# Optimization experiments

Measured on AMD Instinct MI355X. Metric: run time of the kernel, lower is better.

Reference implementation:

```python
import jax, jax.numpy as jnp
import numpy as np

# dims: L=tgt len, S=src len, N=batch, E=embed, H=heads
L, S, N, E, H = 1024, 1024, 4, 1024, 16
HD = E // H  # head dim = 64


def setup_inputs() -> dict:
    key = jax.random.key(0)
    ks = jax.random.split(key, 7)
    w_scale = 0.02
    return {
        "query": jax.random.normal(ks[0], (L, N, E), jnp.float32),
        "key": jax.random.normal(ks[1], (S, N, E), jnp.float32),
        "value": jax.random.normal(ks[2], (S, N, E), jnp.float32),
        "in_proj_weight": jax.random.normal(ks[3], (3 * E, E), jnp.float32) * w_scale,
        "in_proj_bias": jax.random.normal(ks[4], (3 * E,), jnp.float32) * w_scale,
        "out_proj_weight": jax.random.normal(ks[5], (E, E), jnp.float32) * w_scale,
        "out_proj_bias": jax.random.normal(ks[6], (E,), jnp.float32) * w_scale,
    }


def reference(query, key, value, in_proj_weight, in_proj_bias,
              out_proj_weight, out_proj_bias):
    scaling = float(HD) ** -0.5
    # packed QKV projection, sliced exactly as the torch code does
    q = (query @ in_proj_weight[:E].T + in_proj_bias[:E]) * scaling        # (L,N,E)
    k = key @ in_proj_weight[E:2 * E].T + in_proj_bias[E:2 * E]            # (S,N,E)
    v = value @ in_proj_weight[2 * E:].T + in_proj_bias[2 * E:]            # (S,N,E)
    # split heads: (L,N,E) -> (N*H, L, HD)
    q = q.reshape(L, N * H, HD).transpose(1, 0, 2)
    k = k.reshape(S, N * H, HD).transpose(1, 0, 2)
    v = v.reshape(S, N * H, HD).transpose(1, 0, 2)
    scores = jnp.einsum('bld,bsd->bls', q, k)          # (N*H, L, S)
    attn = jax.nn.softmax(scores, axis=-1)
    sig = jax.nn.sigmoid(scores)                        # the need_sigmoid_weights variant
    out = jnp.einsum('bls,bsd->bld', attn, v)          # (N*H, L, HD)
    out = out.transpose(1, 0, 2).reshape(L, N, E)
    out = out @ out_proj_weight.T + out_proj_bias       # (L,N,E)
    # weights averaged over heads, as torch MHA returns: (N,L,S)
    attn_weights = attn.reshape(N, H, L, S).sum(axis=1) / H
    sig_weights = sig.reshape(N, H, L, S).sum(axis=1) / H
    return out, attn_weights, sig_weights
```

## Files before the change

kernel.cpp:

```cpp
#include <hip/hip_runtime.h>

#define L_DIM 1024
#define E_DIM 1024
#define NB 4
#define H_NUM 16
#define HD_DIM 64
#define T_TOK 4096
#define NHB 64

typedef float f32x4 __attribute__((ext_vector_type(4)));
typedef unsigned short u16x8 __attribute__((ext_vector_type(8)));
typedef unsigned short u16x4 __attribute__((ext_vector_type(4)));
typedef __bf16 bf16x8 __attribute__((ext_vector_type(8)));

__device__ inline unsigned short f2bf(float f) {
  unsigned int u = __builtin_bit_cast(unsigned int, f);
  u += 0x7FFFu + ((u >> 16) & 1u);
  return (unsigned short)(u >> 16);
}
__device__ __forceinline__ unsigned int cvt_pk_bf16(float lo, float hi) {
  unsigned int r;
  asm("v_cvt_pk_bf16_f32 %0, %1, %2" : "=v"(r) : "v"(lo), "v"(hi));
  return r;
}
__device__ inline f32x4 mfma16(u16x8 a, u16x8 b, f32x4 c) {
  return __builtin_amdgcn_mfma_f32_16x16x32_bf16(
      __builtin_bit_cast(bf16x8, a), __builtin_bit_cast(bf16x8, b), c, 0, 0, 0);
}

__device__ __forceinline__ void gl2lds16(const void* g, void* l) {
  auto gp = reinterpret_cast<const __attribute__((address_space(1))) unsigned int*>(
      reinterpret_cast<unsigned long long>(g));
  auto lp = reinterpret_cast<__attribute__((address_space(3))) unsigned int*>(
      static_cast<unsigned int>(reinterpret_cast<unsigned long long>(l)));
  __builtin_amdgcn_global_load_lds(gp, lp, 16, 0, 0);
}

__global__ __launch_bounds__(256) void cast_kernel(
    const float* __restrict__ s0, const float* __restrict__ s1,
    const float* __restrict__ s2, const float* __restrict__ s3,
    unsigned short* __restrict__ d0, unsigned short* __restrict__ d1,
    unsigned short* __restrict__ d2, unsigned short* __restrict__ d3,
    int n0, int n1, int n2, int n3) {
  const int y = blockIdx.y;
  const float* s = (y == 0) ? s0 : (y == 1) ? s1 : (y == 2) ? s2 : s3;
  unsigned short* d = (y == 0) ? d0 : (y == 1) ? d1 : (y == 2) ? d2 : d3;
  const int n = (y == 0) ? n0 : (y == 1) ? n1 : (y == 2) ? n2 : n3;
  int idx = (blockIdx.x * 256 + threadIdx.x) * 8;
  const int stride = gridDim.x * 256 * 8;
  for (; idx < n; idx += stride) {
    float4 a = *(const float4*)(s + idx);
    float4 b = *(const float4*)(s + idx + 4);
    u16x8 o = {f2bf(a.x), f2bf(a.y), f2bf(a.z), f2bf(a.w),
               f2bf(b.x), f2bf(b.y), f2bf(b.z), f2bf(b.w)};
    *(u16x8*)(d + idx) = o;
  }
}

__device__ __forceinline__ void stage_tile(const unsigned short* __restrict__ g,
                                           unsigned short* lbuf, int tid) {
  const int r = tid >> 2, c = tid & 3;
  const int sc = c ^ ((r ^ (r >> 2)) & 3);
  gl2lds16(g + (size_t)r * 1024 + sc * 8, lbuf + tid * 8);
  const int r2 = r + 64;
  gl2lds16(g + (size_t)r2 * 1024 + sc * 8, lbuf + (tid + 256) * 8);
}
__device__ __forceinline__ int frag_off(int r, int q) {
  return r * 32 + ((q ^ ((r ^ (r >> 2)) & 3)) << 3);
}

__global__ __launch_bounds__(256) void qkv_gemm(
    const unsigned short* __restrict__ qb, const unsigned short* __restrict__ kb,
    const unsigned short* __restrict__ vb, const unsigned short* __restrict__ Wb,
    const float* __restrict__ bias, unsigned short* __restrict__ q_hm,
    unsigned short* __restrict__ k_hm, unsigned short* __restrict__ v_t) {
  __shared__ __align__(16) unsigned short As[3][4096];
  __shared__ __align__(16) unsigned short Bs[3][4096];
  const int tid = threadIdx.x;
  const int bm = blockIdx.x, bn = blockIdx.y, z = blockIdx.z;
  const unsigned short* Ag = ((z == 0) ? qb : (z == 1) ? kb : vb) + (size_t)bm * 128 * 1024;
  const unsigned short* Bg = Wb + (size_t)z * 1048576 + (size_t)bn * 128 * 1024;
  const float* bc = bias + z * E_DIM;

  const int w = tid >> 6, lane = tid & 63;
  const int wm = w & 1, wn = w >> 1;
  const int quad = lane >> 4, l16 = lane & 15;

  f32x4 acc[4][4];
#pragma unroll
  for (int i = 0; i < 4; i++)
#pragma unroll
    for (int j = 0; j < 4; j++) { f32x4 zz = {0.f, 0.f, 0.f, 0.f}; acc[i][j] = zz; }

  stage_tile(Ag, As[0], tid);
  stage_tile(Bg, Bs[0], tid);

  int cb = 0, sb = 1;
#pragma unroll 1
  for (int kk = 0; kk < 32; kk++) {
    if (kk + 1 < 32) {
      stage_tile(Ag + (kk + 1) * 32, As[sb], tid);
      stage_tile(Bg + (kk + 1) * 32, Bs[sb], tid);
      sb = (sb == 2) ? 0 : sb + 1;
      asm volatile("s_waitcnt vmcnt(4)" ::: "memory");
    } else {
      asm volatile("s_waitcnt vmcnt(0)" ::: "memory");
    }
    __builtin_amdgcn_s_barrier();
    asm volatile("" ::: "memory");
    u16x8 af[4], bfv[4];
#pragma unroll
    for (int mi = 0; mi < 4; mi++) {
      int r = wm * 64 + mi * 16 + l16;
      af[mi] = *(const u16x8*)&As[cb][frag_off(r, quad)];
    }
#pragma unroll
    for (int ni = 0; ni < 4; ni++) {
      int r = wn * 64 + ni * 16 + l16;
      bfv[ni] = *(const u16x8*)&Bs[cb][frag_off(r, quad)];
    }
#pragma unroll
    for (int mi = 0; mi < 4; mi++)
#pragma unroll
      for (int ni = 0; ni < 4; ni++)
        acc[mi][ni] = mfma16(af[mi], bfv[ni], acc[mi][ni]);
    cb = (cb == 2) ? 0 : cb + 1;
  }
#pragma unroll
  for (int ni = 0; ni < 4; ni++) {
    int col = bn * 128 + wn * 64 + ni * 16 + l16;
    float bv = bc[col];
    int h = col >> 6, d = col & 63;
#pragma unroll
    for (int mi = 0; mi < 4; mi++) {
#pragma unroll
      for (int r = 0; r < 4; r++) {
        int t = bm * 128 + wm * 64 + mi * 16 + quad * 4 + r;
        float v = acc[mi][ni][r] + bv;
        int nb = t & 3, pos = t >> 2;
        if (z == 0) {
          v *= 0.125f;
          q_hm[(size_t)((nb * 16 + h) * 1024 + pos) * 64 + d] = f2bf(v);
        } else if (z == 1) {
          k_hm[(size_t)((nb * 16 + h) * 1024 + pos) * 64 + d] = f2bf(v);
        } else {
          v_t[(size_t)((nb * 16 + h) * 64 + d) * 1024 + pos] = f2bf(v);
        }
      }
    }
  }
}

__global__ __launch_bounds__(256, 2) void attn_kernel(
    const unsigned short* __restrict__ q_hm, const unsigned short* __restrict__ k_hm,
    const unsigned short* __restrict__ v_t, unsigned short* __restrict__ o_h,
    float* __restrict__ m_ws, float* __restrict__ r_ws) {
  __shared__ __align__(16) unsigned short stage[6][4096];
  __shared__ __align__(16) unsigned short pt[4][32][68];
  __shared__ float red_m[4][32];
  __shared__ float red_s[4][32];

  const int tid = threadIdx.x;
  const int flat = blockIdx.x + (blockIdx.y << 5);
  const int nf = (flat & 7) * 256 + (flat >> 3);
  const int l0 = (nf & 31) * 32;
  const int b = nf >> 5;
  const int nb = b >> 4, h = b & 15;
  const int w = tid >> 6, lane = tid & 63;
  const int quad = lane >> 4, l16 = lane & 15;

  const int i1 = tid + 256;
  const int r0s = tid >> 3, c0s = tid & 7;
  const int r1s = i1 >> 3, c1s = i1 & 7;
  const int src0 = (c0s ^ (r0s & 7)) * 8;
  const int src1 = (c1s ^ (r1s & 7)) * 8;

  const unsigned short* kbase = k_hm + ((size_t)b << 16);
  const unsigned short* vbase = v_t + ((size_t)b << 16);

  u16x8 bq[2][2];
#pragma unroll
  for (int g = 0; g < 2; g++) {
    const unsigned short* qp =
        q_hm + ((size_t)(b * 1024 + l0 + g * 16 + l16) << 6) + quad * 8;
    bq[g][0] = *(const u16x8*)qp;
    bq[g][1] = *(const u16x8*)(qp + 32);
  }
  asm volatile("" ::: "memory");

  f32x4 acc[16][2];
#pragma unroll
  for (int j = 0; j < 16; j++)
#pragma unroll
    for (int g = 0; g < 2; g++) { f32x4 z = {0.f, 0.f, 0.f, 0.f}; acc[j][g] = z; }

#pragma unroll
  for (int t = 0; t < 4; t++) {
    gl2lds16(kbase + ((size_t)(t * 64 + r0s) << 6) + src0, &stage[t][tid * 8]);
    gl2lds16(kbase + ((size_t)(t * 64 + r1s) << 6) + src1, &stage[t][i1 * 8]);
  }

  const int myrow = w * 16 + l16;
  const int sw0 = ((quad ^ (l16 & 7)) * 8);
  const int sw1 = (((quad + 4) ^ (l16 & 7)) * 8);

#pragma unroll
  for (int i = 0; i < 8; i++) {
    if (i >= 1) {
      const int t0 = 2 * i + 2, t1 = 2 * i + 3;
      if (t0 < 16) {
        gl2lds16(kbase + ((size_t)(t0 * 64 + r0s) << 6) + src0, &stage[t0 % 6][tid * 8]);
        gl2lds16(kbase + ((size_t)(t0 * 64 + r1s) << 6) + src1, &stage[t0 % 6][i1 * 8]);
        gl2lds16(kbase + ((size_t)(t1 * 64 + r0s) << 6) + src0, &stage[t1 % 6][tid * 8]);
        gl2lds16(kbase + ((size_t)(t1 * 64 + r1s) << 6) + src1, &stage[t1 % 6][i1 * 8]);
      } else {
        const int v0 = t0 - 16, v1 = t1 - 16;
        gl2lds16(vbase + ((size_t)r0s << 10) + v0 * 64 + src0, &stage[t0 % 6][tid * 8]);
        gl2lds16(vbase + ((size_t)r1s << 10) + v0 * 64 + src1, &stage[t0 % 6][i1 * 8]);
        gl2lds16(vbase + ((size_t)r0s << 10) + v1 * 64 + src0, &stage[t1 % 6][tid * 8]);
        gl2lds16(vbase + ((size_t)r1s << 10) + v1 * 64 + src1, &stage[t1 % 6][i1 * 8]);
      }
    }
    asm volatile("s_waitcnt vmcnt(4)" ::: "memory");
    __builtin_amdgcn_s_barrier();
    asm volatile("" ::: "memory");
    const int c0 = 2 * i, c1 = 2 * i + 1;
    const unsigned short* kt0 = &stage[c0 % 6][myrow * 64];
    const unsigned short* kt1 = &stage[c1 % 6][myrow * 64];
    u16x8 a00 = *(const u16x8*)(kt0 + sw0);
    u16x8 a01 = *(const u16x8*)(kt0 + sw1);
    u16x8 a10 = *(const u16x8*)(kt1 + sw0);
    u16x8 a11 = *(const u16x8*)(kt1 + sw1);
    acc[c0][0] = mfma16(a00, bq[0][0], acc[c0][0]);
    acc[c0][0] = mfma16(a01, bq[0][1], acc[c0][0]);
    acc[c0][1] = mfma16(a00, bq[1][0], acc[c0][1]);
    acc[c0][1] = mfma16(a01, bq[1][1], acc[c0][1]);
    acc[c1][0] = mfma16(a10, bq[0][0], acc[c1][0]);
    acc[c1][0] = mfma16(a11, bq[0][1], acc[c1][0]);
    acc[c1][1] = mfma16(a10, bq[1][0], acc[c1][1]);
    acc[c1][1] = mfma16(a11, bq[1][1], acc[c1][1]);
  }

  gl2lds16(vbase + ((size_t)r0s << 10) + 2 * 64 + src0, &stage[0][tid * 8]);
  gl2lds16(vbase + ((size_t)r1s << 10) + 2 * 64 + src1, &stage[0][i1 * 8]);
  gl2lds16(vbase + ((size_t)r0s << 10) + 3 * 64 + src0, &stage[1][tid * 8]);
  gl2lds16(vbase + ((size_t)r1s << 10) + 3 * 64 + src1, &stage[1][i1 * 8]);

  float lm0 = -3e38f, lm1 = -3e38f;
#pragma unroll
  for (int j = 0; j < 16; j++)
#pragma unroll
    for (int r = 0; r < 4; r++) {
      lm0 = fmaxf(lm0, acc[j][0][r]);
      lm1 = fmaxf(lm1, acc[j][1][r]);
    }
  lm0 = fmaxf(lm0, __shfl_xor(lm0, 16, 64));
  lm0 = fmaxf(lm0, __shfl_xor(lm0, 32, 64));
  lm1 = fmaxf(lm1, __shfl_xor(lm1, 16, 64));
  lm1 = fmaxf(lm1, __shfl_xor(lm1, 32, 64));
  if (lane < 16) { red_m[w][lane] = lm0; red_m[w][lane + 16] = lm1; }
  asm volatile("s_waitcnt lgkmcnt(0)" ::: "memory");
  __builtin_amdgcn_s_barrier();
  asm volatile("" ::: "memory");
  float m0 = fmaxf(fmaxf(red_m[0][l16], red_m[1][l16]),
                   fmaxf(red_m[2][l16], red_m[3][l16]));
  float m1 = fmaxf(fmaxf(red_m[0][l16 + 16], red_m[1][l16 + 16]),
                   fmaxf(red_m[2][l16 + 16], red_m[3][l16 + 16]));
  float mm = 0.f;
  if (tid < 32)
    mm = fmaxf(fmaxf(red_m[0][tid], red_m[1][tid]),
               fmaxf(red_m[2][tid], red_m[3][tid]));

  float ls0 = 0.f, ls1 = 0.f;
#pragma unroll
  for (int j = 0; j < 16; j++) {
#pragma unroll
    for (int r = 0; r < 4; r++) {
      float e0 = __expf(acc[j][0][r] - m0);
      float e1 = __expf(acc[j][1][r] - m1);
      acc[j][0][r] = e0;
      acc[j][1][r] = e1;
      ls0 += e0;
      ls1 += e1;
    }
  }
  ls0 += __shfl_xor(ls0, 16, 64);
  ls0 += __shfl_xor(ls0, 32, 64);
  ls1 += __shfl_xor(ls1, 16, 64);
  ls1 += __shfl_xor(ls1, 32, 64);
  if (lane < 16) { red_s[w][lane] = ls0; red_s[w][lane + 16] = ls1; }
  asm volatile("s_waitcnt lgkmcnt(0)" ::: "memory");
  __builtin_amdgcn_s_barrier();
  asm volatile("" ::: "memory");
  float rv0 = 1.0f / (red_s[0][l16] + red_s[1][l16] + red_s[2][l16] + red_s[3][l16]);
  float rv1 = 1.0f / (red_s[0][l16 + 16] + red_s[1][l16 + 16] +
                      red_s[2][l16 + 16] + red_s[3][l16 + 16]);
  float ssv = 1.f;
  if (tid < 32)
    ssv = red_s[0][tid] + red_s[1][tid] + red_s[2][tid] + red_s[3][tid];

  {
    uint2 p00 = {cvt_pk_bf16(acc[0][0][0], acc[0][0][1]),
                 cvt_pk_bf16(acc[0][0][2], acc[0][0][3])};
    uint2 p01 = {cvt_pk_bf16(acc[0][1][0], acc[0][1][1]),
                 cvt_pk_bf16(acc[0][1][2], acc[0][1][3])};
    *(uint2*)&pt[0][l16][w * 16 + quad * 4] = p00;
    *(uint2*)&pt[0][16 + l16][w * 16 + quad * 4] = p01;
    uint2 p10 = {cvt_pk_bf16(acc[1][0][0], acc[1][0][1]),
                 cvt_pk_bf16(acc[1][0][2], acc[1][0][3])};
    uint2 p11 = {cvt_pk_bf16(acc[1][1][0], acc[1][1][1]),
                 cvt_pk_bf16(acc[1][1][2], acc[1][1][3])};
    *(uint2*)&pt[1][l16][w * 16 + quad * 4] = p10;
    *(uint2*)&pt[1][16 + l16][w * 16 + quad * 4] = p11;
  }

  f32x4 oacc0 = {0.f, 0.f, 0.f, 0.f};
  f32x4 oacc1 = {0.f, 0.f, 0.f, 0.f};
#pragma unroll
  for (int i = 0; i < 8; i++) {
    if (i >= 1 && i <= 6) {
      const int v0 = 2 * i + 2, v1 = 2 * i + 3;
      const int b0 = (v0 + 16) % 6, b1 = (v1 + 16) % 6;
      gl2lds16(vbase + ((size_t)r0s << 10) + v0 * 64 + src0, &stage[b0][tid * 8]);
      gl2lds16(vbase + ((size_t)r1s << 10) + v0 * 64 + src1, &stage[b0][i1 * 8]);
      gl2lds16(vbase + ((size_t)r0s << 10) + v1 * 64 + src0, &stage[b1][tid * 8]);
      gl2lds16(vbase + ((size_t)r1s << 10) + v1 * 64 + src1, &stage[b1][i1 * 8]);
    }
    if (i < 7) {
      asm volatile("s_waitcnt vmcnt(4) lgkmcnt(0)" ::: "memory");
    } else {
      asm volatile("s_waitcnt vmcnt(0) lgkmcnt(0)" ::: "memory");
    }
    __builtin_amdgcn_s_barrier();
    asm volatile("" ::: "memory");
    if (i < 7) {
      const int tA = 2 * i + 2, tB = 2 * i + 3;
      uint2 pA0 = {cvt_pk_bf16(acc[tA][0][0], acc[tA][0][1]),
                   cvt_pk_bf16(acc[tA][0][2], acc[tA][0][3])};
      uint2 pA1 = {cvt_pk_bf16(acc[tA][1][0], acc[tA][1][1]),
                   cvt_pk_bf16(acc[tA][1][2], acc[tA][1][3])};
      *(uint2*)&pt[tA % 4][l16][w * 16 + quad * 4] = pA0;
      *(uint2*)&pt[tA % 4][16 + l16][w * 16 + quad * 4] = pA1;
      uint2 pB0 = {cvt_pk_bf16(acc[tB][0][0], acc[tB][0][1]),
                   cvt_pk_bf16(acc[tB][0][2], acc[tB][0][3])};
      uint2 pB1 = {cvt_pk_bf16(acc[tB][1][0], acc[tB][1][1]),
                   cvt_pk_bf16(acc[tB][1][2], acc[tB][1][3])};
      *(uint2*)&pt[tB % 4][l16][w * 16 + quad * 4] = pB0;
      *(uint2*)&pt[tB % 4][16 + l16][w * 16 + quad * 4] = pB1;
    }
    const int cA = 2 * i, cB = 2 * i + 1;
    const unsigned short* vt0 = &stage[(cA + 16) % 6][myrow * 64];
    const unsigned short* vt1 = &stage[(cB + 16) % 6][myrow * 64];
    u16x8 bvA0 = *(const u16x8*)(vt0 + sw0);
    u16x8 bvA1 = *(const u16x8*)(vt0 + sw1);
    u16x8 bvB0 = *(const u16x8*)(vt1 + sw0);
    u16x8 bvB1 = *(const u16x8*)(vt1 + sw1);
    u16x8 apA00 = *(const u16x8*)&pt[cA % 4][l16][quad * 8];
    u16x8 apA01 = *(const u16x8*)&pt[cA % 4][l16][32 + quad * 8];
    u16x8 apA10 = *(const u16x8*)&pt[cA % 4][16 + l16][quad * 8];
    u16x8 apA11 = *(const u16x8*)&pt[cA % 4][16 + l16][32 + quad * 8];
    u16x8 apB00 = *(const u16x8*)&pt[cB % 4][l16][quad * 8];
    u16x8 apB01 = *(const u16x8*)&pt[cB % 4][l16][32 + quad * 8];
    u16x8 apB10 = *(const u16x8*)&pt[cB % 4][16 + l16][quad * 8];
    u16x8 apB11 = *(const u16x8*)&pt[cB % 4][16 + l16][32 + quad * 8];
    oacc0 = mfma16(apA00, bvA0, oacc0);
    oacc0 = mfma16(apA01, bvA1, oacc0);
    oacc0 = mfma16(apB00, bvB0, oacc0);
    oacc0 = mfma16(apB01, bvB1, oacc0);
    oacc1 = mfma16(apA10, bvA0, oacc1);
    oacc1 = mfma16(apA11, bvA1, oacc1);
    oacc1 = mfma16(apB10, bvB0, oacc1);
    oacc1 = mfma16(apB11, bvB1, oacc1);
  }

  if (tid < 32) {
    m_ws[b * 1024 + l0 + tid] = mm;
    r_ws[b * 1024 + l0 + tid] = 1.0f / ssv;
  }

#pragma unroll
  for (int r = 0; r < 4; r++) {
    int lr = quad * 4 + r;
    float rr0 = __shfl(rv0, lr, 64);
    float rr1 = __shfl(rv1, lr, 64);
    int t0 = (l0 + lr) * 4 + nb;
    int t1 = (l0 + 16 + lr) * 4 + nb;
    o_h[((size_t)t0 << 10) + h * 64 + w * 16 + l16] = f2bf(oacc0[r] * rr0);
    o_h[((size_t)t1 << 10) + h * 64 + w * 16 + l16] = f2bf(oacc1[r] * rr1);
  }
}

__global__ __launch_bounds__(256, 2) void weights_kernel(
    const unsigned short* __restrict__ q_hm, const unsigned short* __restrict__ k_hm,
    const float* __restrict__ m_ws, const float* __restrict__ r_ws,
    float* __restrict__ attn_out, float* __restrict__ sig_out) {
  __shared__ __align__(16) unsigned short qs[4][4096];
  __shared__ __align__(16) unsigned short ks[4][4096];
  __shared__ float ml[16][64];
  __shared__ float rl[16][64];
  __shared__ float cl[16][64];

  const int tid = threadIdx.x;
  const int flat = blockIdx.x + (blockIdx.y << 4) + (blockIdx.z << 8);
  const int xcd = flat & 7, local = flat >> 3;
  const int nb = xcd >> 1;
  const int idx2 = ((xcd & 1) << 7) + local;
  const int l0 = (idx2 >> 4) << 6;
  const int s0 = (idx2 & 15) << 6;

  const int w = tid >> 6, lane = tid & 63;
  const int quad = lane >> 4, l16 = lane & 15;

  const int i1 = tid + 256;
  const int r0s = tid >> 3, c0s = tid & 7;
  const int r1s = i1 >> 3, c1s = i1 & 7;
  const int src0 = (c0s ^ (r0s & 7)) * 8;
  const int src1 = (c1s ^ (r1s & 7)) * 8;

  {
    int idx = tid * 4;
    int hh = idx >> 6, ii = idx & 63;
    int bb = nb * 16 + hh;
    float4 mv4 = *(const float4*)&m_ws[bb * 1024 + l0 + ii];
    float4 rv4 = *(const float4*)&r_ws[bb * 1024 + l0 + ii];
    *(float4*)&ml[hh][ii] = mv4;
    *(float4*)&rl[hh][ii] = rv4;
    float4 cv4 = {__expf(-mv4.x), __expf(-mv4.y), __expf(-mv4.z), __expf(-mv4.w)};
    *(float4*)&cl[hh][ii] = cv4;
  }

  const int sw0 = ((quad ^ (l16 & 7)) * 8);
  const int sw1 = (((quad + 4) ^ (l16 & 7)) * 8);

  auto stageQK = [&](int h) {
    const int bb = nb * 16 + h;
    const unsigned short* qb = q_hm + ((size_t)(bb * 1024 + l0) << 6);
    const unsigned short* kb = k_hm + ((size_t)(bb * 1024 + s0) << 6);
    const int bf = h & 3;
    gl2lds16(qb + (r0s << 6) + src0, &qs[bf][tid * 8]);
    gl2lds16(qb + (r1s << 6) + src1, &qs[bf][i1 * 8]);
    gl2lds16(kb + (r0s << 6) + src0, &ks[bf][tid * 8]);
    gl2lds16(kb + (r1s << 6) + src1, &ks[bf][i1 * 8]);
  };

  f32x4 accA[4], accS[4];
#pragma unroll
  for (int i = 0; i < 4; i++) {
    f32x4 zz = {0.f, 0.f, 0.f, 0.f};
    accA[i] = zz; accS[i] = zz;
  }

  stageQK(0);
  stageQK(1);
  asm volatile("s_waitcnt lgkmcnt(0)" ::: "memory");

  auto computeH = [&](int h) {
    const int bf = h & 3;
    const unsigned short* qt = &qs[bf][(w * 16 + l16) * 64];
    u16x8 a0 = *(const u16x8*)(qt + sw0);
    u16x8 a1 = *(const u16x8*)(qt + sw1);
    f32x4 mv = *(const f32x4*)&ml[h][w * 16 + quad * 4];
    f32x4 rv = *(const f32x4*)&rl[h][w * 16 + quad * 4];
    f32x4 cv = *(const f32x4*)&cl[h][w * 16 + quad * 4];
#pragma unroll
    for (int ni = 0; ni < 4; ni++) {
      const unsigned short* kt = &ks[bf][(ni * 16 + l16) * 64];
      u16x8 b0 = *(const u16x8*)(kt + sw0);
      u16x8 b1 = *(const u16x8*)(kt + sw1);
      f32x4 scv = {0.f, 0.f, 0.f, 0.f};
      scv = mfma16(a0, b0, scv);
      scv = mfma16(a1, b1, scv);
#pragma unroll
      for (int r = 0; r < 4; r++) {
        float e = __expf(scv[r] - mv[r]);
        accA[ni][r] += e * rv[r];
        accS[ni][r] += e * __builtin_amdgcn_rcpf(e + cv[r]);
      }
    }
  };

#pragma unroll 1
  for (int h = 0; h < 14; ++h) {
    stageQK(h + 2);
    asm volatile("s_waitcnt vmcnt(8)" ::: "memory");
    __builtin_amdgcn_s_barrier();
    asm volatile("" ::: "memory");
    computeH(h);
  }
  asm volatile("s_waitcnt vmcnt(4)" ::: "memory");
  __builtin_amdgcn_s_barrier();
  asm volatile("" ::: "memory");
  computeH(14);
  asm volatile("s_waitcnt vmcnt(0)" ::: "memory");
  __builtin_amdgcn_s_barrier();
  asm volatile("" ::: "memory");
  computeH(15);

  const float inv_h = 1.0f / 16.0f;
  const int lrow0 = l0 + w * 16;
#pragma unroll
  for (int ni = 0; ni < 4; ni++) {
#pragma unroll
    for (int r = 0; r < 4; r++) {
      int l = lrow0 + quad * 4 + r;
      int s = s0 + ni * 16 + l16;
      size_t idx = ((size_t)nb * 1024 + l) * 1024 + s;
      attn_out[idx] = accA[ni][r] * inv_h;
      sig_out[idx] = accS[ni][r] * inv_h;
    }
  }
}

__global__ __launch_bounds__(256) void out_gemm(
    const unsigned short* __restrict__ o_h, const unsigned short* __restrict__ Wb,
    const float* __restrict__ bias, float* __restrict__ out) {
  __shared__ __align__(16) unsigned short As[3][4096];
  __shared__ __align__(16) unsigned short Bs[3][4096];
  const int tid = threadIdx.x;
  const int bm = blockIdx.x, bn = blockIdx.y;
  const unsigned short* Ag = o_h + (size_t)bm * 128 * 1024;
  const unsigned short* Bg = Wb + (size_t)bn * 128 * 1024;

  const int w = tid >> 6, lane = tid & 63;
  const int wm = w & 1, wn = w >> 1;
  const int quad = lane >> 4, l16 = lane & 15;

  f32x4 acc[4][4];
#pragma unroll
  for (int i = 0; i < 4; i++)
#pragma unroll
    for (int j = 0; j < 4; j++) { f32x4 zz = {0.f, 0.f, 0.f, 0.f}; acc[i][j] = zz; }

  stage_tile(Ag, As[0], tid);
  stage_tile(Bg, Bs[0], tid);

  int cb = 0, sb = 1;
#pragma unroll 1
  for (int kk = 0; kk < 32; kk++) {
    if (kk + 1 < 32) {
      stage_tile(Ag + (kk + 1) * 32, As[sb], tid);
      stage_tile(Bg + (kk + 1) * 32, Bs[sb], tid);
      sb = (sb == 2) ? 0 : sb + 1;
      asm volatile("s_waitcnt vmcnt(4)" ::: "memory");
    } else {
      asm volatile("s_waitcnt vmcnt(0)" ::: "memory");
    }
    __builtin_amdgcn_s_barrier();
    asm volatile("" ::: "memory");
    u16x8 af[4], bfv[4];
#pragma unroll
    for (int mi = 0; mi < 4; mi++) {
      int r = wm * 64 + mi * 16 + l16;
      af[mi] = *(const u16x8*)&As[cb][frag_off(r, quad)];
    }
#pragma unroll
    for (int ni = 0; ni < 4; ni++) {
      int r = wn * 64 + ni * 16 + l16;
      bfv[ni] = *(const u16x8*)&Bs[cb][frag_off(r, quad)];
    }
#pragma unroll
    for (int mi = 0; mi < 4; mi++)
#pragma unroll
      for (int ni = 0; ni < 4; ni++)
        acc[mi][ni] = mfma16(af[mi], bfv[ni], acc[mi][ni]);
    cb = (cb == 2) ? 0 : cb + 1;
  }
#pragma unroll
  for (int ni = 0; ni < 4; ni++) {
    int col = bn * 128 + wn * 64 + ni * 16 + l16;
    float bv = bias[col];
#pragma unroll
    for (int mi = 0; mi < 4; mi++) {
#pragma unroll
      for (int r = 0; r < 4; r++) {
        int t = bm * 128 + wm * 64 + mi * 16 + quad * 4 + r;
        out[(size_t)t * E_DIM + col] = acc[mi][ni][r] + bv;
      }
    }
  }
}

extern "C" void kernel_launch(void* const* d_in, const int* in_sizes, int n_in,
                              void* d_out, int out_size, void* d_ws, size_t ws_size,
                              hipStream_t stream) {
  const float* qin  = (const float*)d_in[0];
  const float* kin  = (const float*)d_in[1];
  const float* vin  = (const float*)d_in[2];
  const float* Wqkv = (const float*)d_in[3];
  const float* bqkv = (const float*)d_in[4];
  const float* Wout = (const float*)d_in[5];
  const float* bout = (const float*)d_in[6];
  float* out      = (float*)d_out;
  float* attn_out = out + 4194304;
  float* sig_out  = out + 8388608;

  unsigned short* q_hm = (unsigned short*)d_ws;
  unsigned short* k_hm = q_hm + 4194304;
  unsigned short* v_t  = q_hm + 8388608;
  unsigned short* o_h  = q_hm + 12582912;
  float* m_ws = (float*)(q_hm + 16777216);
  float* r_ws = m_ws + 65536;

  unsigned short* qb = (unsigned short*)(out + 4194304);
  unsigned short* kb = qb + 4194304;
  unsigned short* vb = qb + 8388608;
  unsigned short* Wqkvb = o_h;
  unsigned short* Woutb = v_t;

  cast_kernel<<<dim3(2048, 4), 256, 0, stream>>>(
      qin, kin, vin, Wqkv, qb, kb, vb, Wqkvb,
      4194304, 4194304, 4194304, 3145728);
  qkv_gemm<<<dim3(32, 8, 3), 256, 0, stream>>>(qb, kb, vb, Wqkvb, bqkv,
                                               q_hm, k_hm, v_t);
  attn_kernel<<<dim3(32, 64), 256, 0, stream>>>(q_hm, k_hm, v_t, o_h, m_ws, r_ws);
  cast_kernel<<<dim3(512, 1), 256, 0, stream>>>(
      Wout, Wout, Wout, Wout, Woutb, Woutb, Woutb, Woutb,
      1048576, 0, 0, 0);
  weights_kernel<<<dim3(16, 16, 4), 256, 0, stream>>>(q_hm, k_hm, m_ws, r_ws,
                                                      attn_out, sig_out);
  out_gemm<<<dim3(32, 8), 256, 0, stream>>>(o_h, Woutb, bout, out);
}
```

Measured before the change: 251.5 us.

## Defer softmax exp into PV loop and pair-pipeline heads in weights kernel

In the attention kernel, the exponentials are now computed just in time per tile inside the P·V loop, and the row-sum reduction with its barrier moves after the loop. This interleaves exp work with MFMAs and removes a barrier before the PV phase. In the weights kernel, heads are now processed two per iteration with one full wait and barrier per pair, halving the barrier count. The cost is shallower prefetch depth, since each wait now drains all outstanding loads instead of keeping some in flight.

Measured after the change: 250.4 us. Within noise of the previous version (-0.4%).

```diff
diff --git a/kernel.cpp b/kernel.cpp
--- a/kernel.cpp
+++ b/kernel.cpp
@@ -272,47 +272,20 @@
                fmaxf(red_m[2][tid], red_m[3][tid]));
 
   float ls0 = 0.f, ls1 = 0.f;
-#pragma unroll
-  for (int j = 0; j < 16; j++) {
-#pragma unroll
-    for (int r = 0; r < 4; r++) {
-      float e0 = __expf(acc[j][0][r] - m0);
-      float e1 = __expf(acc[j][1][r] - m1);
-      acc[j][0][r] = e0;
-      acc[j][1][r] = e1;
-      ls0 += e0;
-      ls1 += e1;
-    }
-  }
-  ls0 += __shfl_xor(ls0, 16, 64);
-  ls0 += __shfl_xor(ls0, 32, 64);
-  ls1 += __shfl_xor(ls1, 16, 64);
-  ls1 += __shfl_xor(ls1, 32, 64);
-  if (lane < 16) { red_s[w][lane] = ls0; red_s[w][lane + 16] = ls1; }
-  asm volatile("s_waitcnt lgkmcnt(0)" ::: "memory");
-  __builtin_amdgcn_s_barrier();
-  asm volatile("" ::: "memory");
-  float rv0 = 1.0f / (red_s[0][l16] + red_s[1][l16] + red_s[2][l16] + red_s[3][l16]);
-  float rv1 = 1.0f / (red_s[0][l16 + 16] + red_s[1][l16 + 16] +
-                      red_s[2][l16 + 16] + red_s[3][l16 + 16]);
-  float ssv = 1.f;
-  if (tid < 32)
-    ssv = red_s[0][tid] + red_s[1][tid] + red_s[2][tid] + red_s[3][tid];
-
-  {
-    uint2 p00 = {cvt_pk_bf16(acc[0][0][0], acc[0][0][1]),
-                 cvt_pk_bf16(acc[0][0][2], acc[0][0][3])};
-    uint2 p01 = {cvt_pk_bf16(acc[0][1][0], acc[0][1][1]),
-                 cvt_pk_bf16(acc[0][1][2], acc[0][1][3])};
-    *(uint2*)&pt[0][l16][w * 16 + quad * 4] = p00;
-    *(uint2*)&pt[0][16 + l16][w * 16 + quad * 4] = p01;
-    uint2 p10 = {cvt_pk_bf16(acc[1][0][0], acc[1][0][1]),
-                 cvt_pk_bf16(acc[1][0][2], acc[1][0][3])};
-    uint2 p11 = {cvt_pk_bf16(acc[1][1][0], acc[1][1][1]),
-                 cvt_pk_bf16(acc[1][1][2], acc[1][1][3])};
-    *(uint2*)&pt[1][l16][w * 16 + quad * 4] = p10;
-    *(uint2*)&pt[1][16 + l16][w * 16 + quad * 4] = p11;
-  }
+  auto exppk = [&](int t, int slot) {
+    float e0a = __expf(acc[t][0][0] - m0), e0b = __expf(acc[t][0][1] - m0);
+    float e0c = __expf(acc[t][0][2] - m0), e0d = __expf(acc[t][0][3] - m0);
+    float e1a = __expf(acc[t][1][0] - m1), e1b = __expf(acc[t][1][1] - m1);
+    float e1c = __expf(acc[t][1][2] - m1), e1d = __expf(acc[t][1][3] - m1);
+    ls0 += (e0a + e0b) + (e0c + e0d);
+    ls1 += (e1a + e1b) + (e1c + e1d);
+    uint2 p0 = {cvt_pk_bf16(e0a, e0b), cvt_pk_bf16(e0c, e0d)};
+    uint2 p1 = {cvt_pk_bf16(e1a, e1b), cvt_pk_bf16(e1c, e1d)};
+    *(uint2*)&pt[slot][l16][w * 16 + quad * 4] = p0;
+    *(uint2*)&pt[slot][16 + l16][w * 16 + quad * 4] = p1;
+  };
+  exppk(0, 0);
+  exppk(1, 1);
 
   f32x4 oacc0 = {0.f, 0.f, 0.f, 0.f};
   f32x4 oacc1 = {0.f, 0.f, 0.f, 0.f};
@@ -334,19 +307,8 @@
     __builtin_amdgcn_s_barrier();
     asm volatile("" ::: "memory");
     if (i < 7) {
-      const int tA = 2 * i + 2, tB = 2 * i + 3;
-      uint2 pA0 = {cvt_pk_bf16(acc[tA][0][0], acc[tA][0][1]),
-                   cvt_pk_bf16(acc[tA][0][2], acc[tA][0][3])};
-      uint2 pA1 = {cvt_pk_bf16(acc[tA][1][0], acc[tA][1][1]),
-                   cvt_pk_bf16(acc[tA][1][2], acc[tA][1][3])};
-      *(uint2*)&pt[tA % 4][l16][w * 16 + quad * 4] = pA0;
-      *(uint2*)&pt[tA % 4][16 + l16][w * 16 + quad * 4] = pA1;
-      uint2 pB0 = {cvt_pk_bf16(acc[tB][0][0], acc[tB][0][1]),
-                   cvt_pk_bf16(acc[tB][0][2], acc[tB][0][3])};
-      uint2 pB1 = {cvt_pk_bf16(acc[tB][1][0], acc[tB][1][1]),
-                   cvt_pk_bf16(acc[tB][1][2], acc[tB][1][3])};
-      *(uint2*)&pt[tB % 4][l16][w * 16 + quad * 4] = pB0;
-      *(uint2*)&pt[tB % 4][16 + l16][w * 16 + quad * 4] = pB1;
+      exppk(2 * i + 2, (2 * i + 2) % 4);
+      exppk(2 * i + 3, (2 * i + 3) % 4);
     }
     const int cA = 2 * i, cB = 2 * i + 1;
     const unsigned short* vt0 = &stage[(cA + 16) % 6][myrow * 64];
@@ -373,7 +335,19 @@
     oacc1 = mfma16(apB11, bvB1, oacc1);
   }
 
+  ls0 += __shfl_xor(ls0, 16, 64);
+  ls0 += __shfl_xor(ls0, 32, 64);
+  ls1 += __shfl_xor(ls1, 16, 64);
+  ls1 += __shfl_xor(ls1, 32, 64);
+  if (lane < 16) { red_s[w][lane] = ls0; red_s[w][lane + 16] = ls1; }
+  asm volatile("s_waitcnt lgkmcnt(0)" ::: "memory");
+  __builtin_amdgcn_s_barrier();
+  asm volatile("" ::: "memory");
+  float rv0 = 1.0f / (red_s[0][l16] + red_s[1][l16] + red_s[2][l16] + red_s[3][l16]);
+  float rv1 = 1.0f / (red_s[0][l16 + 16] + red_s[1][l16 + 16] +
+                      red_s[2][l16 + 16] + red_s[3][l16 + 16]);
   if (tid < 32) {
+    float ssv = red_s[0][tid] + red_s[1][tid] + red_s[2][tid] + red_s[3][tid];
     m_ws[b * 1024 + l0 + tid] = mm;
     r_ws[b * 1024 + l0 + tid] = 1.0f / ssv;
   }
@@ -452,7 +426,6 @@
 
   stageQK(0);
   stageQK(1);
-  asm volatile("s_waitcnt lgkmcnt(0)" ::: "memory");
 
   auto computeH = [&](int h) {
     const int bf = h & 3;
@@ -480,21 +453,17 @@
   };
 
 #pragma unroll 1
-  for (int h = 0; h < 14; ++h) {
-    stageQK(h + 2);
-    asm volatile("s_waitcnt vmcnt(8)" ::: "memory");
+  for (int p = 0; p < 8; ++p) {
+    asm volatile("s_waitcnt vmcnt(0) lgkmcnt(0)" ::: "memory");
     __builtin_amdgcn_s_barrier();
     asm volatile("" ::: "memory");
-    computeH(h);
-  }
-  asm volatile("s_waitcnt vmcnt(4)" ::: "memory");
-  __builtin_amdgcn_s_barrier();
-  asm volatile("" ::: "memory");
-  computeH(14);
-  asm volatile("s_waitcnt vmcnt(0)" ::: "memory");
-  __builtin_amdgcn_s_barrier();
-  asm volatile("" ::: "memory");
-  computeH(15);
+    if (p < 7) {
+      stageQK(2 * p + 2);
+      stageQK(2 * p + 3);
+    }
+    computeH(2 * p);
+    computeH(2 * p + 1);
+  }
 
   const float inv_h = 1.0f / 16.0f;
   const int lrow0 = l0 + w * 16;
```
